# Optimization experiments

Hardware: AMD Instinct MI355X
Metric: run time of the kernel (lower is better)

The kernel has to match this reference:

```python
import jax, jax.numpy as jnp
import numpy as np

NUM_HEADS = 16
HEAD_DIM = 64

def setup_inputs() -> dict:
    key = jax.random.key(0)
    k1, k2, k3 = jax.random.split(key, 3)
    B, S, H = 2, 2048, 1024
    inner = NUM_HEADS * HEAD_DIM  # 1024
    x = jax.random.normal(k1, (B, S, H), dtype=jnp.float32)
    w_qkv = jax.random.normal(k2, (H, 3 * inner), dtype=jnp.float32) * (1.0 / np.sqrt(H))
    b_qkv = jnp.zeros((3 * inner,), dtype=jnp.float32)
    w_out = jax.random.normal(k3, (inner, H), dtype=jnp.float32) * (1.0 / np.sqrt(inner))
    b_out = jnp.zeros((H,), dtype=jnp.float32)
    return {"x": x, "w_qkv": w_qkv, "b_qkv": b_qkv, "w_out": w_out, "b_out": b_out}

def reference(x, w_qkv, b_qkv, w_out, b_out):
    B, S, H = x.shape
    nh, hd = NUM_HEADS, HEAD_DIM
    qkv = x @ w_qkv + b_qkv                      # [B,S,3*nh*hd]
    qkv = qkv.reshape(B, S, 3, nh, hd)
    qkv = jnp.transpose(qkv, (2, 0, 3, 1, 4))    # [3,B,nh,S,hd]
    q, k, v = qkv[0], qkv[1], qkv[2]
    scale = jnp.sqrt(jnp.asarray(hd, dtype=x.dtype))
    attn = jnp.einsum('bhqd,bhkd->bhqk', q, k) / scale  # [B,nh,S,S]
    attn = jax.nn.softmax(attn, axis=-1)
    out = jnp.einsum('bhqk,bhkd->bhqd', attn, v)        # [B,nh,S,hd]
    out = jnp.transpose(out, (0, 2, 1, 3)).reshape(B, S, nh * hd)
    out = out @ w_out + b_out                    # [B,S,H]
    return out
```

## Files before the change

kernel.cpp:

```cpp
#include <hip/hip_runtime.h>
#include <stdint.h>

typedef short bf16x8 __attribute__((ext_vector_type(8)));
typedef float f32x4 __attribute__((ext_vector_type(4)));

#if __has_builtin(__builtin_amdgcn_exp2f)
#define EXP2F(x) __builtin_amdgcn_exp2f(x)
#else
#define EXP2F(x) exp2f(x)
#endif

#define QSCALE 0.18033688011112042f

__device__ __forceinline__ unsigned short f2bf(float f) {
  unsigned u = __float_as_uint(f);
  u += 0x7fffu + ((u >> 16) & 1u);
  return (unsigned short)(u >> 16);
}

__device__ __forceinline__ unsigned cvtpk(float lo, float hi) {
  unsigned r;
  asm("v_cvt_pk_bf16_f32 %0, %1, %2" : "=v"(r) : "v"(lo), "v"(hi));
  return r;
}

__device__ __forceinline__ void pl32(unsigned& a, unsigned& b) {
  asm("v_permlane32_swap_b32 %0, %1" : "+v"(a), "+v"(b));
}
__device__ __forceinline__ void pl16(unsigned& a, unsigned& b) {
  asm("v_permlane16_swap_b32 %0, %1" : "+v"(a), "+v"(b));
}

__device__ __forceinline__ void gld16(const ushort* g, ushort* l) {
  __builtin_amdgcn_global_load_lds(
      (__attribute__((address_space(1))) void*)g,
      (__attribute__((address_space(3))) void*)l, 16, 0, 0);
}

__global__ __launch_bounds__(256) void k_cast_bf16(const float* __restrict__ in,
                                                   ushort* __restrict__ out) {
  int i = (blockIdx.x * 256 + threadIdx.x) * 8;
  float4 a = *(const float4*)(in + i);
  float4 b = *(const float4*)(in + i + 4);
  union { ushort u[8]; uint4 q; } r;
  r.u[0] = f2bf(a.x); r.u[1] = f2bf(a.y); r.u[2] = f2bf(a.z); r.u[3] = f2bf(a.w);
  r.u[4] = f2bf(b.x); r.u[5] = f2bf(b.y); r.u[6] = f2bf(b.z); r.u[7] = f2bf(b.w);
  *(uint4*)(out + i) = r.q;
}

__global__ __launch_bounds__(256) void k_transpose_cast(const float* __restrict__ in,
                                                        ushort* __restrict__ out,
                                                        int R, int C) {
  __shared__ float tl[32][33];
  int t = threadIdx.x;
  {
    int r = t >> 3, c4 = (t & 7) * 4;
    float4 v = *(const float4*)(in + (size_t)(blockIdx.y * 32 + r) * C + blockIdx.x * 32 + c4);
    tl[r][c4] = v.x; tl[r][c4 + 1] = v.y; tl[r][c4 + 2] = v.z; tl[r][c4 + 3] = v.w;
  }
  __syncthreads();
  {
    int c = t >> 3, r4 = (t & 7) * 4;
    union { ushort u[4]; uint2 q; } o;
    o.u[0] = f2bf(tl[r4][c]);     o.u[1] = f2bf(tl[r4 + 1][c]);
    o.u[2] = f2bf(tl[r4 + 2][c]); o.u[3] = f2bf(tl[r4 + 3][c]);
    *(uint2*)(out + (size_t)(blockIdx.x * 32 + c) * R + blockIdx.y * 32 + r4) = o.q;
  }
}

__global__ __launch_bounds__(256, 2) void k_gemm_qkv(
    const ushort* __restrict__ A, const ushort* __restrict__ Bt,
    const float* __restrict__ bias, ushort* __restrict__ Q,
    ushort* __restrict__ Ko, ushort* __restrict__ Vt) {
  __shared__ ushort As[2][128 * 32];
  __shared__ ushort Bs[2][128 * 32];
  const int t = threadIdx.x;
  const int lane = t & 63, wid = t >> 6;
  const int wr = wid >> 1, wc = wid & 1;
  const int rt = blockIdx.y, ct = blockIdx.x;

  const int srow = t >> 2, sslot = t & 3;
  const ushort* ga = A + (size_t)(rt * 128 + srow) * 1024 + sslot * 8;
  const ushort* gb = Bt + (size_t)(ct * 128 + srow) * 1024 + sslot * 8;

  f32x4 acc[4][4];
#pragma unroll
  for (int m = 0; m < 4; ++m)
#pragma unroll
    for (int n = 0; n < 4; ++n) acc[m][n] = (f32x4){0.f, 0.f, 0.f, 0.f};

  int aidx[4], bidx[4];
#pragma unroll
  for (int m = 0; m < 4; ++m) {
    int ra = wr * 64 + m * 16 + (lane & 15);
    aidx[m] = ra * 32 + ((lane >> 4) << 3);
    int rb = wc * 64 + m * 16 + (lane & 15);
    bidx[m] = rb * 32 + ((lane >> 4) << 3);
  }

  gld16(ga, &As[0][t * 8]); gld16(ga + 65536, &As[0][2048 + t * 8]);
  gld16(gb, &Bs[0][t * 8]); gld16(gb + 65536, &Bs[0][2048 + t * 8]);
  __syncthreads();

  int cur = 0;
  for (int kt = 0; kt < 32; ++kt) {
    if (kt < 31) {
      const ushort* ga2 = ga + (kt + 1) * 32;
      const ushort* gb2 = gb + (kt + 1) * 32;
      gld16(ga2, &As[cur ^ 1][t * 8]); gld16(ga2 + 65536, &As[cur ^ 1][2048 + t * 8]);
      gld16(gb2, &Bs[cur ^ 1][t * 8]); gld16(gb2 + 65536, &Bs[cur ^ 1][2048 + t * 8]);
    }
    bf16x8 af[4], bfv[4];
#pragma unroll
    for (int m = 0; m < 4; ++m) af[m] = *(const bf16x8*)&As[cur][aidx[m]];
#pragma unroll
    for (int n = 0; n < 4; ++n) bfv[n] = *(const bf16x8*)&Bs[cur][bidx[n]];
#pragma unroll
    for (int m = 0; m < 4; ++m)
#pragma unroll
      for (int n = 0; n < 4; ++n)
        acc[m][n] = __builtin_amdgcn_mfma_f32_16x16x32_bf16(af[m], bfv[n], acc[m][n], 0, 0, 0);
    __syncthreads();
    cur ^= 1;
  }

  const int colb = ct * 128 + wc * 64;
  const int rowb = rt * 128 + wr * 64;
#pragma unroll
  for (int n = 0; n < 4; ++n) {
    int col = colb + n * 16 + (lane & 15);
    float bv = bias[col];
    int three = col >> 10, hx = (col >> 6) & 15, d = col & 63;
    if (three == 2) {
#pragma unroll
      for (int m = 0; m < 4; ++m) {
        int r0 = rowb + m * 16 + ((lane >> 4) << 2);
        int b = r0 >> 11, s0 = r0 & 2047;
        int s0p = (s0 & ~56) | (((s0 >> 3) ^ d) & 7) << 3;
        union { ushort u[4]; uint2 q; } o;
#pragma unroll
        for (int r = 0; r < 4; ++r) o.u[r] = f2bf(acc[m][n][r] + bv);
        *(uint2*)&Vt[(size_t)(b * 16 + hx) * 131072 + (size_t)d * 2048 + s0p] = o.q;
      }
    } else if (three == 1) {
#pragma unroll
      for (int m = 0; m < 4; ++m) {
        int r0 = rowb + m * 16 + ((lane >> 4) << 2);
#pragma unroll
        for (int r = 0; r < 4; ++r) {
          int row = r0 + r;
          int b = row >> 11, s = row & 2047;
          int dp = (d & 7) | ((((d >> 3) ^ s) & 7) << 3);
          Ko[(size_t)((b * 16 + hx) * 2048 + s) * 64 + dp] = f2bf(acc[m][n][r] + bv);
        }
      }
    } else {
#pragma unroll
      for (int m = 0; m < 4; ++m) {
        int r0 = rowb + m * 16 + ((lane >> 4) << 2);
#pragma unroll
        for (int r = 0; r < 4; ++r) {
          int row = r0 + r;
          int b = row >> 11, s = row & 2047;
          Q[(size_t)((b * 16 + hx) * 2048 + s) * 64 + d] = f2bf((acc[m][n][r] + bv) * QSCALE);
        }
      }
    }
  }
}

__global__ __launch_bounds__(256, 2) void k_gemm_out(
    const ushort* __restrict__ A, const ushort* __restrict__ Bt,
    const float* __restrict__ bias, float* __restrict__ Out) {
  __shared__ ushort As[2][64 * 32];
  __shared__ ushort Bs[2][128 * 32];
  const int t = threadIdx.x;
  const int lane = t & 63, wid = t >> 6;
  const int wr = wid >> 1, wc = wid & 1;
  const int rt = blockIdx.y, ct = blockIdx.x;

  const int srow = t >> 2, sslot = t & 3;
  const ushort* ga = A + (size_t)(rt * 64 + srow) * 1024 + sslot * 8;
  const ushort* gb = Bt + (size_t)(ct * 128 + srow) * 1024 + sslot * 8;

  f32x4 acc[2][4];
#pragma unroll
  for (int m = 0; m < 2; ++m)
#pragma unroll
    for (int n = 0; n < 4; ++n) acc[m][n] = (f32x4){0.f, 0.f, 0.f, 0.f};

  int aidx[2], bidx[4];
#pragma unroll
  for (int m = 0; m < 2; ++m) {
    int ra = wr * 32 + m * 16 + (lane & 15);
    aidx[m] = ra * 32 + ((lane >> 4) << 3);
  }
#pragma unroll
  for (int n = 0; n < 4; ++n) {
    int rb = wc * 64 + n * 16 + (lane & 15);
    bidx[n] = rb * 32 + ((lane >> 4) << 3);
  }

  gld16(ga, &As[0][t * 8]);
  gld16(gb, &Bs[0][t * 8]); gld16(gb + 65536, &Bs[0][2048 + t * 8]);
  __syncthreads();

  int cur = 0;
  for (int kt = 0; kt < 32; ++kt) {
    if (kt < 31) {
      const ushort* ga2 = ga + (kt + 1) * 32;
      const ushort* gb2 = gb + (kt + 1) * 32;
      gld16(ga2, &As[cur ^ 1][t * 8]);
      gld16(gb2, &Bs[cur ^ 1][t * 8]); gld16(gb2 + 65536, &Bs[cur ^ 1][2048 + t * 8]);
    }
    bf16x8 af[2], bfv[4];
#pragma unroll
    for (int m = 0; m < 2; ++m) af[m] = *(const bf16x8*)&As[cur][aidx[m]];
#pragma unroll
    for (int n = 0; n < 4; ++n) bfv[n] = *(const bf16x8*)&Bs[cur][bidx[n]];
#pragma unroll
    for (int m = 0; m < 2; ++m)
#pragma unroll
      for (int n = 0; n < 4; ++n)
        acc[m][n] = __builtin_amdgcn_mfma_f32_16x16x32_bf16(af[m], bfv[n], acc[m][n], 0, 0, 0);
    __syncthreads();
    cur ^= 1;
  }

  const int colb = ct * 128 + wc * 64;
  const int rowb = rt * 64 + wr * 32;
#pragma unroll
  for (int n = 0; n < 4; ++n) {
    int col = colb + n * 16 + (lane & 15);
    float bv = bias[col];
#pragma unroll
    for (int m = 0; m < 2; ++m) {
      int r0 = rowb + m * 16 + ((lane >> 4) << 2);
#pragma unroll
      for (int r = 0; r < 4; ++r)
        Out[(size_t)(r0 + r) * 1024 + col] = acc[m][n][r] + bv;
    }
  }
}

__global__ __launch_bounds__(256, 2) void k_attn(const ushort* __restrict__ Qb,
                                                 const ushort* __restrict__ Kb,
                                                 const ushort* __restrict__ Vtb,
                                                 ushort* __restrict__ AO) {
  __shared__ ushort Ks[2][64 * 64];
  __shared__ ushort Vs[2][64 * 64];
  const int t = threadIdx.x, lane = t & 63, wid = t >> 6;
  const int c = lane & 15, g = lane >> 4;
  const int bh = blockIdx.y, qt = blockIdx.x;
  const ushort* Qh = Qb + (size_t)bh * 131072;
  const ushort* Kh = Kb + (size_t)bh * 131072;
  const ushort* Vh = Vtb + (size_t)bh * 131072;

  bf16x8 qf[2][2];
#pragma unroll
  for (int cb = 0; cb < 2; ++cb)
#pragma unroll
    for (int kk = 0; kk < 2; ++kk) {
      int row = qt * 128 + wid * 32 + cb * 16 + c;
      qf[cb][kk] = *(const bf16x8*)&Qh[row * 64 + kk * 32 + g * 8];
    }

  f32x4 oacc[2][4];
#pragma unroll
  for (int cb = 0; cb < 2; ++cb)
#pragma unroll
    for (int n = 0; n < 4; ++n) oacc[cb][n] = (f32x4){0.f, 0.f, 0.f, 0.f};
  float lpart[2] = {0.f, 0.f};

  const int strow = lane >> 3, stch = (lane & 7) * 8;

  int kidx[4][2];
#pragma unroll
  for (int n = 0; n < 4; ++n)
#pragma unroll
    for (int kk = 0; kk < 2; ++kk)
      kidx[n][kk] = (n * 16 + c) * 64 + (((kk * 4 + g) ^ (c & 7)) << 3);

#pragma unroll
  for (int i = 0; i < 2; ++i) {
    int row = (wid * 2 + i) * 8 + strow;
    gld16(&Kh[(size_t)row * 64 + stch], &Ks[0][(wid * 2 + i) * 512 + lane * 8]);
    gld16(&Vh[(size_t)row * 2048 + stch], &Vs[0][(wid * 2 + i) * 512 + lane * 8]);
  }
  __syncthreads();

  int cur = 0;
  for (int kt = 0; kt < 32; ++kt) {
    if (kt < 31) {
#pragma unroll
      for (int i = 0; i < 2; ++i) {
        int row = (wid * 2 + i) * 8 + strow;
        gld16(&Kh[(size_t)((kt + 1) * 64 + row) * 64 + stch],
              &Ks[cur ^ 1][(wid * 2 + i) * 512 + lane * 8]);
        gld16(&Vh[(size_t)row * 2048 + (kt + 1) * 64 + stch],
              &Vs[cur ^ 1][(wid * 2 + i) * 512 + lane * 8]);
      }
    }
    const ushort* Kc = &Ks[cur][0];
    const ushort* Vc = &Vs[cur][0];
    f32x4 sacc[2][4];
#pragma unroll
    for (int cb = 0; cb < 2; ++cb)
#pragma unroll
      for (int n = 0; n < 4; ++n) sacc[cb][n] = (f32x4){0.f, 0.f, 0.f, 0.f};
    __builtin_amdgcn_s_setprio(1);
#pragma unroll
    for (int kk = 0; kk < 2; ++kk)
#pragma unroll
      for (int n = 0; n < 4; ++n) {
        bf16x8 kf = *(const bf16x8*)&Kc[kidx[n][kk]];
        sacc[0][n] = __builtin_amdgcn_mfma_f32_16x16x32_bf16(kf, qf[0][kk], sacc[0][n], 0, 0, 0);
        sacc[1][n] = __builtin_amdgcn_mfma_f32_16x16x32_bf16(kf, qf[1][kk], sacc[1][n], 0, 0, 0);
      }
    __builtin_amdgcn_s_setprio(0);
    uint2 W[2][4];
#pragma unroll
    for (int cb = 0; cb < 2; ++cb) {
      float ps = lpart[cb];
#pragma unroll
      for (int n = 0; n < 4; ++n) {
        float p0 = EXP2F(sacc[cb][n][0] - 16.0f);
        float p1 = EXP2F(sacc[cb][n][1] - 16.0f);
        float p2 = EXP2F(sacc[cb][n][2] - 16.0f);
        float p3 = EXP2F(sacc[cb][n][3] - 16.0f);
        ps += (p0 + p1) + (p2 + p3);
        W[cb][n].x = cvtpk(p0, p1);
        W[cb][n].y = cvtpk(p2, p3);
      }
      lpart[cb] = ps;
    }
    __builtin_amdgcn_s_setprio(1);
#pragma unroll
    for (int kk = 0; kk < 2; ++kk) {
      bf16x8 paf[2];
#pragma unroll
      for (int cb = 0; cb < 2; ++cb) {
        unsigned a0 = W[cb][2 * kk].x, b0 = W[cb][2 * kk + 1].x;
        pl32(a0, b0); pl16(a0, b0);
        unsigned a1 = W[cb][2 * kk].y, b1 = W[cb][2 * kk + 1].y;
        pl32(a1, b1); pl16(a1, b1);
        union { unsigned u[4]; bf16x8 v; } fr;
        fr.u[0] = a0; fr.u[1] = a1; fr.u[2] = b0; fr.u[3] = b1;
        paf[cb] = fr.v;
      }
#pragma unroll
      for (int nd = 0; nd < 4; ++nd) {
        bf16x8 vf = *(const bf16x8*)&Vc[kidx[nd][kk]];
        oacc[0][nd] = __builtin_amdgcn_mfma_f32_16x16x32_bf16(paf[0], vf, oacc[0][nd], 0, 0, 0);
        oacc[1][nd] = __builtin_amdgcn_mfma_f32_16x16x32_bf16(paf[1], vf, oacc[1][nd], 0, 0, 0);
      }
    }
    __builtin_amdgcn_s_setprio(0);
    __syncthreads();
    cur ^= 1;
  }

  const int b = bh >> 4, h = bh & 15;
#pragma unroll
  for (int cb = 0; cb < 2; ++cb) {
    float lp = lpart[cb];
    lp += __shfl_xor(lp, 16);
    lp += __shfl_xor(lp, 32);
    float inv = 1.0f / lp;
    float invr[4];
#pragma unroll
    for (int r = 0; r < 4; ++r) invr[r] = __shfl(inv, (g << 2) + r);
#pragma unroll
    for (int nd = 0; nd < 4; ++nd) {
      int d = nd * 16 + c;
#pragma unroll
      for (int r = 0; r < 4; ++r) {
        int s = qt * 128 + wid * 32 + cb * 16 + (g << 2) + r;
        AO[(size_t)((b * 2048 + s) * 16 + h) * 64 + d] = f2bf(oacc[cb][nd][r] * invr[r]);
      }
    }
  }
}

extern "C" void kernel_launch(void* const* d_in, const int* in_sizes, int n_in,
                              void* d_out, int out_size, void* d_ws, size_t ws_size,
                              hipStream_t stream) {
  const float* x = (const float*)d_in[0];
  const float* w_qkv = (const float*)d_in[1];
  const float* b_qkv = (const float*)d_in[2];
  const float* w_out = (const float*)d_in[3];
  const float* b_out = (const float*)d_in[4];
  float* out = (float*)d_out;

  char* p = (char*)d_ws;
  ushort* xb = (ushort*)p;    p += (size_t)4096 * 1024 * 2;
  ushort* wqkvT = (ushort*)p; p += (size_t)3072 * 1024 * 2;
  ushort* woutT = (ushort*)p; p += (size_t)1024 * 1024 * 2;
  ushort* Qb = (ushort*)p;    p += (size_t)32 * 2048 * 64 * 2;
  ushort* Kb = (ushort*)p;    p += (size_t)32 * 2048 * 64 * 2;
  ushort* Vtb = (ushort*)p;   p += (size_t)32 * 2048 * 64 * 2;
  ushort* AO = xb;

  k_cast_bf16<<<2048, 256, 0, stream>>>(x, xb);
  k_transpose_cast<<<dim3(96, 32), 256, 0, stream>>>(w_qkv, wqkvT, 1024, 3072);
  k_transpose_cast<<<dim3(32, 32), 256, 0, stream>>>(w_out, woutT, 1024, 1024);
  k_gemm_qkv<<<dim3(24, 32), 256, 0, stream>>>(xb, wqkvT, b_qkv, Qb, Kb, Vtb);
  k_attn<<<dim3(16, 32), 256, 0, stream>>>(Qb, Kb, Vtb, AO);
  k_gemm_out<<<dim3(8, 64), 256, 0, stream>>>(AO, woutT, b_out, out);
}
```

Before: 116.5 us.

## Software-pipeline QK^T one tile ahead with triple-buffered K/V, merge prep kernels

The attention loop now uses three LDS buffers for K and V and computes the next tile's QK^T scores while the current tile's softmax and PV MFMAs run, so the exp work can overlap matrix-core work. Two S accumulator sets alternate, and the loop is unrolled by two. Separately, the three cast and transpose kernels are merged into one launch with block-index dispatch to save launch overhead. This raises register use and LDS footprint (48KB per block), which may hurt occupancy at two blocks per CU.

Result: faster. 109.5 us, median of 3 (-6.0%).

```diff
diff --git a/kernel.cpp b/kernel.cpp
--- a/kernel.cpp
+++ b/kernel.cpp
@@ -37,25 +37,35 @@
       (__attribute__((address_space(3))) void*)l, 16, 0, 0);
 }
 
-__global__ __launch_bounds__(256) void k_cast_bf16(const float* __restrict__ in,
-                                                   ushort* __restrict__ out) {
-  int i = (blockIdx.x * 256 + threadIdx.x) * 8;
-  float4 a = *(const float4*)(in + i);
-  float4 b = *(const float4*)(in + i + 4);
-  union { ushort u[8]; uint4 q; } r;
-  r.u[0] = f2bf(a.x); r.u[1] = f2bf(a.y); r.u[2] = f2bf(a.z); r.u[3] = f2bf(a.w);
-  r.u[4] = f2bf(b.x); r.u[5] = f2bf(b.y); r.u[6] = f2bf(b.z); r.u[7] = f2bf(b.w);
-  *(uint4*)(out + i) = r.q;
-}
-
-__global__ __launch_bounds__(256) void k_transpose_cast(const float* __restrict__ in,
-                                                        ushort* __restrict__ out,
-                                                        int R, int C) {
+__global__ __launch_bounds__(256) void k_prep(
+    const float* __restrict__ x, ushort* __restrict__ xb,
+    const float* __restrict__ wqkv, ushort* __restrict__ wqkvT,
+    const float* __restrict__ wout, ushort* __restrict__ woutT) {
   __shared__ float tl[32][33];
-  int t = threadIdx.x;
+  const int t = threadIdx.x;
+  const int blk = blockIdx.x;
+  if (blk < 2048) {
+    int i = (blk * 256 + t) * 8;
+    float4 a = *(const float4*)(x + i);
+    float4 b = *(const float4*)(x + i + 4);
+    union { ushort u[8]; uint4 q; } r;
+    r.u[0] = f2bf(a.x); r.u[1] = f2bf(a.y); r.u[2] = f2bf(a.z); r.u[3] = f2bf(a.w);
+    r.u[4] = f2bf(b.x); r.u[5] = f2bf(b.y); r.u[6] = f2bf(b.z); r.u[7] = f2bf(b.w);
+    *(uint4*)(xb + i) = r.q;
+    return;
+  }
+  const float* in; ushort* out; int C, bx, by;
+  if (blk < 5120) {
+    int b = blk - 2048; bx = b % 96; by = b / 96;
+    in = wqkv; out = wqkvT; C = 3072;
+  } else {
+    int b = blk - 5120; bx = b & 31; by = b >> 5;
+    in = wout; out = woutT; C = 1024;
+  }
+  const int R = 1024;
   {
     int r = t >> 3, c4 = (t & 7) * 4;
-    float4 v = *(const float4*)(in + (size_t)(blockIdx.y * 32 + r) * C + blockIdx.x * 32 + c4);
+    float4 v = *(const float4*)(in + (size_t)(by * 32 + r) * C + bx * 32 + c4);
     tl[r][c4] = v.x; tl[r][c4 + 1] = v.y; tl[r][c4 + 2] = v.z; tl[r][c4 + 3] = v.w;
   }
   __syncthreads();
@@ -64,7 +74,7 @@
     union { ushort u[4]; uint2 q; } o;
     o.u[0] = f2bf(tl[r4][c]);     o.u[1] = f2bf(tl[r4 + 1][c]);
     o.u[2] = f2bf(tl[r4 + 2][c]); o.u[3] = f2bf(tl[r4 + 3][c]);
-    *(uint2*)(out + (size_t)(blockIdx.x * 32 + c) * R + blockIdx.y * 32 + r4) = o.q;
+    *(uint2*)(out + (size_t)(bx * 32 + c) * R + by * 32 + r4) = o.q;
   }
 }
 
@@ -243,12 +253,86 @@
   }
 }
 
+#define QKT_COMPUTE(KSRC, SD)                                                 \
+  {                                                                           \
+    _Pragma("unroll")                                                         \
+    for (int cb = 0; cb < 2; ++cb)                                            \
+      _Pragma("unroll")                                                       \
+      for (int n = 0; n < 4; ++n) SD[cb][n] = (f32x4){0.f, 0.f, 0.f, 0.f};    \
+    __builtin_amdgcn_s_setprio(1);                                            \
+    _Pragma("unroll")                                                         \
+    for (int kk = 0; kk < 2; ++kk)                                            \
+      _Pragma("unroll")                                                       \
+      for (int n = 0; n < 4; ++n) {                                           \
+        bf16x8 kf = *(const bf16x8*)&(KSRC)[kidx[n][kk]];                     \
+        SD[0][n] = __builtin_amdgcn_mfma_f32_16x16x32_bf16(kf, qf[0][kk], SD[0][n], 0, 0, 0); \
+        SD[1][n] = __builtin_amdgcn_mfma_f32_16x16x32_bf16(kf, qf[1][kk], SD[1][n], 0, 0, 0); \
+      }                                                                       \
+    __builtin_amdgcn_s_setprio(0);                                            \
+  }
+
+#define ATTN_ITER(T, SCUR, SNXT)                                              \
+  {                                                                           \
+    if ((T) < 30) {                                                           \
+      _Pragma("unroll")                                                       \
+      for (int i = 0; i < 2; ++i) {                                           \
+        int row = (wid * 2 + i) * 8 + strow;                                  \
+        gld16(&Kh[(size_t)(((T) + 2) * 64 + row) * 64 + stch],                \
+              Kstg + (wid * 2 + i) * 512 + lane * 8);                         \
+        gld16(&Vh[(size_t)row * 2048 + ((T) + 2) * 64 + stch],                \
+              Vstg + (wid * 2 + i) * 512 + lane * 8);                         \
+      }                                                                       \
+    }                                                                         \
+    if ((T) < 31) QKT_COMPUTE(Knxt, SNXT);                                    \
+    uint2 W[2][4];                                                            \
+    _Pragma("unroll")                                                         \
+    for (int cb = 0; cb < 2; ++cb) {                                          \
+      float ps = lpart[cb];                                                   \
+      _Pragma("unroll")                                                       \
+      for (int n = 0; n < 4; ++n) {                                           \
+        float p0 = EXP2F(SCUR[cb][n][0] - 16.0f);                             \
+        float p1 = EXP2F(SCUR[cb][n][1] - 16.0f);                             \
+        float p2 = EXP2F(SCUR[cb][n][2] - 16.0f);                             \
+        float p3 = EXP2F(SCUR[cb][n][3] - 16.0f);                             \
+        ps += (p0 + p1) + (p2 + p3);                                          \
+        W[cb][n].x = cvtpk(p0, p1);                                           \
+        W[cb][n].y = cvtpk(p2, p3);                                           \
+      }                                                                       \
+      lpart[cb] = ps;                                                         \
+    }                                                                         \
+    __builtin_amdgcn_s_setprio(1);                                            \
+    _Pragma("unroll")                                                         \
+    for (int kk = 0; kk < 2; ++kk) {                                          \
+      bf16x8 paf[2];                                                          \
+      _Pragma("unroll")                                                       \
+      for (int cb = 0; cb < 2; ++cb) {                                        \
+        unsigned a0 = W[cb][2 * kk].x, b0 = W[cb][2 * kk + 1].x;              \
+        pl32(a0, b0); pl16(a0, b0);                                           \
+        unsigned a1 = W[cb][2 * kk].y, b1 = W[cb][2 * kk + 1].y;              \
+        pl32(a1, b1); pl16(a1, b1);                                           \
+        union { unsigned u[4]; bf16x8 v; } fr;                                \
+        fr.u[0] = a0; fr.u[1] = a1; fr.u[2] = b0; fr.u[3] = b1;               \
+        paf[cb] = fr.v;                                                       \
+      }                                                                       \
+      _Pragma("unroll")                                                       \
+      for (int nd = 0; nd < 4; ++nd) {                                        \
+        bf16x8 vf = *(const bf16x8*)&Vcur[kidx[nd][kk]];                      \
+        oacc[0][nd] = __builtin_amdgcn_mfma_f32_16x16x32_bf16(paf[0], vf, oacc[0][nd], 0, 0, 0); \
+        oacc[1][nd] = __builtin_amdgcn_mfma_f32_16x16x32_bf16(paf[1], vf, oacc[1][nd], 0, 0, 0); \
+      }                                                                       \
+    }                                                                         \
+    __builtin_amdgcn_s_setprio(0);                                            \
+    __syncthreads();                                                          \
+    { ushort* tk = Kcur; Kcur = Knxt; Knxt = Kstg; Kstg = tk;                 \
+      ushort* tv = Vcur; Vcur = Vnxt; Vnxt = Vstg; Vstg = tv; }               \
+  }
+
 __global__ __launch_bounds__(256, 2) void k_attn(const ushort* __restrict__ Qb,
                                                  const ushort* __restrict__ Kb,
                                                  const ushort* __restrict__ Vtb,
                                                  ushort* __restrict__ AO) {
-  __shared__ ushort Ks[2][64 * 64];
-  __shared__ ushort Vs[2][64 * 64];
+  __shared__ ushort Ks[3][64 * 64];
+  __shared__ ushort Vs[3][64 * 64];
   const int t = threadIdx.x, lane = t & 63, wid = t >> 6;
   const int c = lane & 15, g = lane >> 4;
   const int bh = blockIdx.y, qt = blockIdx.x;
@@ -281,83 +365,25 @@
     for (int kk = 0; kk < 2; ++kk)
       kidx[n][kk] = (n * 16 + c) * 64 + (((kk * 4 + g) ^ (c & 7)) << 3);
 
+  ushort *Kcur = &Ks[0][0], *Knxt = &Ks[1][0], *Kstg = &Ks[2][0];
+  ushort *Vcur = &Vs[0][0], *Vnxt = &Vs[1][0], *Vstg = &Vs[2][0];
+
 #pragma unroll
   for (int i = 0; i < 2; ++i) {
     int row = (wid * 2 + i) * 8 + strow;
-    gld16(&Kh[(size_t)row * 64 + stch], &Ks[0][(wid * 2 + i) * 512 + lane * 8]);
-    gld16(&Vh[(size_t)row * 2048 + stch], &Vs[0][(wid * 2 + i) * 512 + lane * 8]);
+    gld16(&Kh[(size_t)row * 64 + stch], Kcur + (wid * 2 + i) * 512 + lane * 8);
+    gld16(&Vh[(size_t)row * 2048 + stch], Vcur + (wid * 2 + i) * 512 + lane * 8);
+    gld16(&Kh[(size_t)(64 + row) * 64 + stch], Knxt + (wid * 2 + i) * 512 + lane * 8);
+    gld16(&Vh[(size_t)row * 2048 + 64 + stch], Vnxt + (wid * 2 + i) * 512 + lane * 8);
   }
   __syncthreads();
 
-  int cur = 0;
-  for (int kt = 0; kt < 32; ++kt) {
-    if (kt < 31) {
-#pragma unroll
-      for (int i = 0; i < 2; ++i) {
-        int row = (wid * 2 + i) * 8 + strow;
-        gld16(&Kh[(size_t)((kt + 1) * 64 + row) * 64 + stch],
-              &Ks[cur ^ 1][(wid * 2 + i) * 512 + lane * 8]);
-        gld16(&Vh[(size_t)row * 2048 + (kt + 1) * 64 + stch],
-              &Vs[cur ^ 1][(wid * 2 + i) * 512 + lane * 8]);
-      }
-    }
-    const ushort* Kc = &Ks[cur][0];
-    const ushort* Vc = &Vs[cur][0];
-    f32x4 sacc[2][4];
-#pragma unroll
-    for (int cb = 0; cb < 2; ++cb)
-#pragma unroll
-      for (int n = 0; n < 4; ++n) sacc[cb][n] = (f32x4){0.f, 0.f, 0.f, 0.f};
-    __builtin_amdgcn_s_setprio(1);
-#pragma unroll
-    for (int kk = 0; kk < 2; ++kk)
-#pragma unroll
-      for (int n = 0; n < 4; ++n) {
-        bf16x8 kf = *(const bf16x8*)&Kc[kidx[n][kk]];
-        sacc[0][n] = __builtin_amdgcn_mfma_f32_16x16x32_bf16(kf, qf[0][kk], sacc[0][n], 0, 0, 0);
-        sacc[1][n] = __builtin_amdgcn_mfma_f32_16x16x32_bf16(kf, qf[1][kk], sacc[1][n], 0, 0, 0);
-      }
-    __builtin_amdgcn_s_setprio(0);
-    uint2 W[2][4];
-#pragma unroll
-    for (int cb = 0; cb < 2; ++cb) {
-      float ps = lpart[cb];
-#pragma unroll
-      for (int n = 0; n < 4; ++n) {
-        float p0 = EXP2F(sacc[cb][n][0] - 16.0f);
-        float p1 = EXP2F(sacc[cb][n][1] - 16.0f);
-        float p2 = EXP2F(sacc[cb][n][2] - 16.0f);
-        float p3 = EXP2F(sacc[cb][n][3] - 16.0f);
-        ps += (p0 + p1) + (p2 + p3);
-        W[cb][n].x = cvtpk(p0, p1);
-        W[cb][n].y = cvtpk(p2, p3);
-      }
-      lpart[cb] = ps;
-    }
-    __builtin_amdgcn_s_setprio(1);
-#pragma unroll
-    for (int kk = 0; kk < 2; ++kk) {
-      bf16x8 paf[2];
-#pragma unroll
-      for (int cb = 0; cb < 2; ++cb) {
-        unsigned a0 = W[cb][2 * kk].x, b0 = W[cb][2 * kk + 1].x;
-        pl32(a0, b0); pl16(a0, b0);
-        unsigned a1 = W[cb][2 * kk].y, b1 = W[cb][2 * kk + 1].y;
-        pl32(a1, b1); pl16(a1, b1);
-        union { unsigned u[4]; bf16x8 v; } fr;
-        fr.u[0] = a0; fr.u[1] = a1; fr.u[2] = b0; fr.u[3] = b1;
-        paf[cb] = fr.v;
-      }
-#pragma unroll
-      for (int nd = 0; nd < 4; ++nd) {
-        bf16x8 vf = *(const bf16x8*)&Vc[kidx[nd][kk]];
-        oacc[0][nd] = __builtin_amdgcn_mfma_f32_16x16x32_bf16(paf[0], vf, oacc[0][nd], 0, 0, 0);
-        oacc[1][nd] = __builtin_amdgcn_mfma_f32_16x16x32_bf16(paf[1], vf, oacc[1][nd], 0, 0, 0);
-      }
-    }
-    __builtin_amdgcn_s_setprio(0);
-    __syncthreads();
-    cur ^= 1;
+  f32x4 sA[2][4], sB[2][4];
+  QKT_COMPUTE(Kcur, sA);
+
+  for (int kt = 0; kt < 32; kt += 2) {
+    ATTN_ITER(kt, sA, sB);
+    ATTN_ITER(kt + 1, sB, sA);
   }
 
   const int b = bh >> 4, h = bh & 15;
@@ -401,9 +427,7 @@
   ushort* Vtb = (ushort*)p;   p += (size_t)32 * 2048 * 64 * 2;
   ushort* AO = xb;
 
-  k_cast_bf16<<<2048, 256, 0, stream>>>(x, xb);
-  k_transpose_cast<<<dim3(96, 32), 256, 0, stream>>>(w_qkv, wqkvT, 1024, 3072);
-  k_transpose_cast<<<dim3(32, 32), 256, 0, stream>>>(w_out, woutT, 1024, 1024);
+  k_prep<<<6144, 256, 0, stream>>>(x, xb, w_qkv, wqkvT, w_out, woutT);
   k_gemm_qkv<<<dim3(24, 32), 256, 0, stream>>>(xb, wqkvT, b_qkv, Qb, Kb, Vtb);
   k_attn<<<dim3(16, 32), 256, 0, stream>>>(Qb, Kb, Vtb, AO);
   k_gemm_out<<<dim3(8, 64), 256, 0, stream>>>(AO, woutT, b_out, out);
```
